# Kernel tuning notes

Measured on AMD Instinct MI355X. Metric: run time of the kernel, lower is better.

Reference implementation:

```python
import jax, jax.numpy as jnp
import numpy as np

B, S, D = 4, 4096, 1024
H, R = 16, 256
HD = D // H  # 64

def setup_inputs() -> dict:
    key = jax.random.key(0)
    ks = jax.random.split(key, 10)
    s = 1.0 / np.sqrt(D)
    return {
        "x": jax.random.normal(ks[0], (B, S, D), dtype=jnp.float32),
        "wq": jax.random.normal(ks[1], (D, D), dtype=jnp.float32) * s,
        "bq": jnp.zeros((D,), dtype=jnp.float32),
        "wk": jax.random.normal(ks[2], (D, D), dtype=jnp.float32) * s,
        "bk": jnp.zeros((D,), dtype=jnp.float32),
        "wv": jax.random.normal(ks[3], (D, D), dtype=jnp.float32) * s,
        "bv": jnp.zeros((D,), dtype=jnp.float32),
        "wo": jax.random.normal(ks[4], (D, D), dtype=jnp.float32) * s,
        "bo": jnp.zeros((D,), dtype=jnp.float32),
        "random_features": jax.random.normal(ks[5], (H, HD, R), dtype=jnp.float32),
    }

def reference(x, wq, bq, wk, bk, wv, bv, wo, bo, random_features):
    b, s, _ = x.shape
    # projections (torch Linear: x @ W.T + b) -> [b, h, s, hd]
    def proj(w, bias):
        return (x @ w.T + bias).reshape(b, s, H, HD).transpose(0, 2, 1, 3)
    q = proj(wq, bq)
    k = proj(wk, bk)
    v = proj(wv, bv)
    # random feature maps: [b,h,s,r]
    q_prime = jnp.exp(jnp.einsum('bhsd,hdr->bhsr', q, random_features)
                      - 0.5 * jnp.sum(q * q, axis=-1, keepdims=True))
    k_prime = jnp.exp(jnp.einsum('bhsd,hdr->bhsr', k, random_features)
                      - 0.5 * jnp.sum(k * k, axis=-1, keepdims=True))
    # kv aggregation: [b,h,r,hd]
    kv_prime = jnp.einsum('bhsr,bhsd->bhrd', k_prime, v)
    attn = jnp.einsum('bhsr,bhrd->bhsd', q_prime, kv_prime)
    # normalization: [b,h,s,1]
    norm = jnp.einsum('bhsr,bhr->bhs', q_prime, jnp.sum(k_prime, axis=-2))[..., None]
    attn = attn / (norm + 1e-6)
    attn = attn.transpose(0, 2, 1, 3).reshape(b, s, D)
    return attn @ wo.T + bo
```

## Files before the change

### kernel.cpp

```cpp
#include <hip/hip_runtime.h>
#include <stdint.h>

#define B_  4
#define S_  4096
#define D_  1024
#define H_  16
#define R_  256
#define HD_ 64
#define BH_ 64
#define M_  16384
#define SPLITK_ 8

typedef uint16_t u16;
typedef __attribute__((ext_vector_type(8))) short short8;
typedef __attribute__((ext_vector_type(4))) float f32x4;
typedef __attribute__((ext_vector_type(4))) unsigned short us4;

__device__ __forceinline__ u16 f2bf(float f){
  union { float f; uint32_t u; } v; v.f = f;
  uint32_t r = v.u + 0x7FFFu + ((v.u >> 16) & 1u);
  return (u16)(r >> 16);
}
__device__ __forceinline__ float bf2f(u16 h){
  union { uint32_t u; float f; } v; v.u = ((uint32_t)h) << 16;
  return v.f;
}
__device__ __forceinline__ f32x4 mfma16(short8 a, short8 b, f32x4 c){
  return __builtin_amdgcn_mfma_f32_16x16x32_bf16(a, b, c, 0, 0, 0);
}
__device__ __forceinline__ void gl_lds16(const u16* g, u16* l){
  __builtin_amdgcn_global_load_lds((const __attribute__((address_space(1))) void*)g,
                                   (__attribute__((address_space(3))) void*)l, 16, 0, 0);
}
__device__ __forceinline__ void cvt8(const float4& a, const float4& b, short8& hi, short8& lo){
  float f[8] = {a.x,a.y,a.z,a.w,b.x,b.y,b.z,b.w};
  #pragma unroll
  for (int j=0;j<8;j++){
    u16 h = f2bf(f[j]);
    hi[j] = (short)h;
    lo[j] = (short)f2bf(f[j] - bf2f(h));
  }
}

__device__ __forceinline__ void stage_rf_full(const u16* __restrict__ rfh,
                                              const u16* __restrict__ rfl,
                                              int h, int tid, int w,
                                              u16* lrfh, u16* lrfl){
  const u16* baseH = rfh + (size_t)h*(R_*HD_);
  const u16* baseL = rfl + (size_t)h*(R_*HD_);
  #pragma unroll
  for (int c=0;c<8;c++){
    int idx = c*256 + tid;
    int row = idx >> 3, gd = idx & 7;
    int gs  = gd ^ (row & 7);
    gl_lds16(baseH + row*64 + gs*8, lrfh + c*2048 + w*512);
    gl_lds16(baseL + row*64 + gs*8, lrfl + c*2048 + w*512);
  }
}

__device__ __forceinline__ void stage_rf_half(const u16* __restrict__ rfh,
                                              const u16* __restrict__ rfl,
                                              int h, int th, int tid, int w,
                                              u16* lrfh, u16* lrfl){
  const u16* baseH = rfh + (size_t)h*(R_*HD_) + (size_t)th*128*HD_;
  const u16* baseL = rfl + (size_t)h*(R_*HD_) + (size_t)th*128*HD_;
  #pragma unroll
  for (int c=0;c<4;c++){
    int idx = c*256 + tid;
    int row = idx >> 3, gd = idx & 7;
    int gs  = gd ^ (row & 7);
    gl_lds16(baseH + row*64 + gs*8, lrfh + c*2048 + w*512);
    gl_lds16(baseL + row*64 + gs*8, lrfl + c*2048 + w*512);
  }
}

__global__ void split_kernel(const float* __restrict__ src, u16* __restrict__ hi,
                             u16* __restrict__ lo, int n4){
  int i = blockIdx.x*blockDim.x + threadIdx.x;
  if (i >= n4) return;
  float4 f = ((const float4*)src)[i];
  float ff[4] = {f.x,f.y,f.z,f.w};
  us4 hv, lv;
  #pragma unroll
  for (int j=0;j<4;j++){
    u16 h = f2bf(ff[j]);
    hv[j] = h;
    lv[j] = f2bf(ff[j] - bf2f(h));
  }
  ((us4*)hi)[i] = hv;
  if (lo) ((us4*)lo)[i] = lv;
}

__global__ void rf_split_kernel(const float* __restrict__ rf, u16* __restrict__ rhi,
                                u16* __restrict__ rlo){
  int idx = blockIdx.x*256 + threadIdx.x;
  int d = idx & 63, r = (idx >> 6) & 255, h = idx >> 14;
  float f = rf[((size_t)h*HD_ + d)*R_ + r];
  u16 hh = f2bf(f);
  rhi[idx] = hh;
  rlo[idx] = f2bf(f - bf2f(hh));
}

__device__ __forceinline__ void rowsq(const float4& x0, const float4& x1,
                                      const float4& x2, const float4& x3,
                                      int q, float sql[4]){
  float s = x0.x*x0.x + x0.y*x0.y + x0.z*x0.z + x0.w*x0.w
          + x1.x*x1.x + x1.y*x1.y + x1.z*x1.z + x1.w*x1.w
          + x2.x*x2.x + x2.y*x2.y + x2.z*x2.z + x2.w*x2.w
          + x3.x*x3.x + x3.y*x3.y + x3.z*x3.z + x3.w*x3.w;
  s += __shfl_xor(s, 16);
  s += __shfl_xor(s, 32);
  #pragma unroll
  for (int r4=0;r4<4;r4++) sql[r4] = 0.5f * __shfl(s, q*4 + r4);
}

template<int NSPLIT, int EPI>
__global__ __launch_bounds__(256, 2)
void gemm128(const u16* __restrict__ Ah, const u16* __restrict__ Al,
             const u16* __restrict__ Bh, const u16* __restrict__ Bl,
             const float* __restrict__ bias, float* __restrict__ outF,
             u16* __restrict__ outB){
  constexpr int NBUF = (NSPLIT==3) ? 4 : 2;
  __shared__ u16 lds[NBUF * 4096];
  const int tid = threadIdx.x, w = tid >> 6, lane = tid & 63;
  const int wm = w & 1, wn = w >> 1;
  const int m0 = blockIdx.x * 128, n0 = blockIdx.y * 128;
  const int q = lane >> 4, rr = lane & 15;

  const int c0 = w*2, c1 = w*2 + 1;
  const int row0 = c0*16 + (lane >> 2), row1 = c1*16 + (lane >> 2);
  const int g0 = (lane & 3) ^ ((row0 >> 1) & 3);
  const int g1 = (lane & 3) ^ ((row1 >> 1) & 3);
  const size_t a0 = (size_t)(m0 + row0)*1024 + g0*8;
  const size_t a1 = (size_t)(m0 + row1)*1024 + g1*8;
  const size_t b0 = (size_t)(n0 + row0)*1024 + g0*8;
  const size_t b1 = (size_t)(n0 + row1)*1024 + g1*8;

  f32x4 acc[4][4];
  #pragma unroll
  for (int i=0;i<4;i++)
    #pragma unroll
    for (int j=0;j<4;j++) acc[i][j] = f32x4{0.f,0.f,0.f,0.f};

  for (int kt=0; kt<32; kt++){
    const int k0 = kt*32;
    gl_lds16(Ah + a0 + k0, lds + 0*4096 + c0*512);
    gl_lds16(Ah + a1 + k0, lds + 0*4096 + c1*512);
    gl_lds16(Bh + b0 + k0, lds + 1*4096 + c0*512);
    gl_lds16(Bh + b1 + k0, lds + 1*4096 + c1*512);
    if constexpr (NSPLIT == 3){
      gl_lds16(Al + a0 + k0, lds + 2*4096 + c0*512);
      gl_lds16(Al + a1 + k0, lds + 2*4096 + c1*512);
      gl_lds16(Bl + b0 + k0, lds + 3*4096 + c0*512);
      gl_lds16(Bl + b1 + k0, lds + 3*4096 + c1*512);
    }
    __syncthreads();

    short8 afh[4], bfh[4], afl[4], bfl[4];
    #pragma unroll
    for (int i=0;i<4;i++){
      int r  = wm*64 + i*16 + rr;
      int o  = r*32 + ((q ^ ((r >> 1) & 3))*8);
      afh[i] = *(const short8*)(lds + 0*4096 + o);
      if constexpr (NSPLIT == 3) afl[i] = *(const short8*)(lds + 2*4096 + o);
      int rn = wn*64 + i*16 + rr;
      int on = rn*32 + ((q ^ ((rn >> 1) & 3))*8);
      bfh[i] = *(const short8*)(lds + 1*4096 + on);
      if constexpr (NSPLIT == 3) bfl[i] = *(const short8*)(lds + 3*4096 + on);
    }
    #pragma unroll
    for (int i=0;i<4;i++)
      #pragma unroll
      for (int j=0;j<4;j++){
        acc[i][j] = mfma16(afh[i], bfh[j], acc[i][j]);
        if constexpr (NSPLIT == 3){
          acc[i][j] = mfma16(afh[i], bfl[j], acc[i][j]);
          acc[i][j] = mfma16(afl[i], bfh[j], acc[i][j]);
        }
      }
    __syncthreads();
  }

  #pragma unroll
  for (int i=0;i<4;i++){
    #pragma unroll
    for (int j=0;j<4;j++){
      int n  = n0 + wn*64 + j*16 + rr;
      float bb = bias[n];
      if constexpr (EPI == 1){
        int mb = m0 + wm*64 + i*16 + q*4;
        us4 pk;
        #pragma unroll
        for (int r4=0;r4<4;r4++) pk[r4] = f2bf(acc[i][j][r4] + bb);
        *(us4*)(outB + ((size_t)((mb >> 12)*H_ + (n >> 6))*HD_ + (n & 63))*S_ + (mb & 4095)) = pk;
      } else {
        #pragma unroll
        for (int r4=0;r4<4;r4++){
          int m = m0 + wm*64 + i*16 + q*4 + r4;
          float v = acc[i][j][r4] + bb;
          if constexpr (EPI == 0)
            outF[((size_t)((m >> 12)*H_ + (n >> 6)))*S_*HD_ + (size_t)(m & 4095)*HD_ + (n & 63)] = v;
          else
            outF[(size_t)m*1024 + n] = v;
        }
      }
    }
  }
}

__global__ __launch_bounds__(256, 1)
void kfeat_kv_kernel(const float* __restrict__ k32,
                     const u16* __restrict__ rfh, const u16* __restrict__ rfl,
                     const u16* __restrict__ vt, u16* __restrict__ kvp16){
  __shared__ u16 kp[128*72];
  __shared__ u16 lrfh[128*HD_];
  __shared__ u16 lrfl[128*HD_];
  const int sp = blockIdx.x, hb = blockIdx.y, th = blockIdx.z, h = hb & 15;
  const int tid = threadIdx.x, w = tid >> 6, lane = tid & 63;
  const int q = lane >> 4, rr = lane & 15;
  const int sw8 = rr & 7;

  stage_rf_half(rfh, rfl, h, th, tid, w, lrfh, lrfl);

  short8 ones;
  { u16 one = (rr == 0) ? (u16)0x3F80 : (u16)0;
    #pragma unroll
    for (int j=0;j<8;j++) ones[j] = (short)one; }

  f32x4 acc2[2][5];
  #pragma unroll
  for (int a=0;a<2;a++)
    #pragma unroll
    for (int t=0;t<5;t++) acc2[a][t] = f32x4{0.f,0.f,0.f,0.f};

  __syncthreads();

  const float* ap0 = k32 + ((size_t)hb*S_ + sp*(S_/SPLITK_) + w*16 + rr)*HD_ + q*8;
  float4 x0 = *(const float4*)(ap0);
  float4 x1 = *(const float4*)(ap0 + 4);
  float4 x2 = *(const float4*)(ap0 + 32);
  float4 x3 = *(const float4*)(ap0 + 36);

  for (int sub=0; sub<(S_/SPLITK_)/64; sub++){
    const int s0 = sp*(S_/SPLITK_) + sub*64;
    float sql[4];
    rowsq(x0, x1, x2, x3, q, sql);
    short8 ah[2], al[2];
    cvt8(x0, x1, ah[0], al[0]);
    cvt8(x2, x3, ah[1], al[1]);
    if (sub < (S_/SPLITK_)/64 - 1){
      const float* apn = k32 + ((size_t)hb*S_ + s0 + 64 + w*16 + rr)*HD_ + q*8;
      x0 = *(const float4*)(apn);
      x1 = *(const float4*)(apn + 4);
      x2 = *(const float4*)(apn + 32);
      x3 = *(const float4*)(apn + 36);
    }

    f32x4 accp[8];
    #pragma unroll
    for (int tt=0;tt<8;tt++) accp[tt] = f32x4{0.f,0.f,0.f,0.f};
    #pragma unroll
    for (int tt=0;tt<8;tt++){
      const u16* lrow  = lrfh + (tt*16 + rr)*64;
      const u16* lrowl = lrfl + (tt*16 + rr)*64;
      short8 bh0 = *(const short8*)(lrow  + ((q     ^ sw8))*8);
      short8 bh1 = *(const short8*)(lrow  + (((q+4) ^ sw8))*8);
      short8 bl0 = *(const short8*)(lrowl + ((q     ^ sw8))*8);
      short8 bl1 = *(const short8*)(lrowl + (((q+4) ^ sw8))*8);
      f32x4 c = accp[tt];
      c = mfma16(ah[0], bh0, c); c = mfma16(ah[0], bl0, c); c = mfma16(al[0], bh0, c);
      c = mfma16(ah[1], bh1, c); c = mfma16(ah[1], bl1, c); c = mfma16(al[1], bh1, c);
      accp[tt] = c;
    }
    #pragma unroll
    for (int tt=0;tt<8;tt++){
      us4 pk;
      #pragma unroll
      for (int r4=0;r4<4;r4++) pk[r4] = f2bf(__expf(accp[tt][r4] - sql[r4]));
      *(us4*)(kp + (tt*16 + rr)*72 + w*16 + q*4) = pk;
    }
    __syncthreads();
    #pragma unroll
    for (int ks=0; ks<2; ks++){
      short8 af[2];
      #pragma unroll
      for (int a=0;a<2;a++)
        af[a] = *(const short8*)(kp + (w*32 + a*16 + rr)*72 + ks*32 + q*8);
      #pragma unroll
      for (int t=0;t<5;t++){
        short8 bf;
        if (t < 4)
          bf = *(const short8*)(vt + ((size_t)hb*HD_ + t*16 + rr)*S_ + s0 + ks*32 + q*8);
        else
          bf = ones;
        #pragma unroll
        for (int a=0;a<2;a++) acc2[a][t] = mfma16(af[a], bf, acc2[a][t]);
      }
    }
    __syncthreads();
  }
  u16* op = kvp16 + ((size_t)hb*SPLITK_ + sp)*R_*80;
  #pragma unroll
  for (int a=0;a<2;a++)
    #pragma unroll
    for (int t=0;t<5;t++)
      #pragma unroll
      for (int r4=0;r4<4;r4++){
        int r = th*128 + w*32 + a*16 + q*4 + r4;
        int c = t*16 + rr;
        op[r*80 + c] = f2bf(acc2[a][t][r4]);
      }
}

__global__ void kv_reduce_kernel(const u16* __restrict__ kvp16, u16* __restrict__ kvt,
                                 float* __restrict__ ksum){
  int r = blockIdx.x, hb = blockIdx.y, c = threadIdx.x;
  if (c >= 65) return;
  const u16* base = kvp16 + (size_t)hb*SPLITK_*R_*80 + r*80 + c;
  float s = 0.f;
  #pragma unroll
  for (int sp=0; sp<SPLITK_; sp++) s += bf2f(base[(size_t)sp*R_*80]);
  if (c < 64) kvt[((size_t)hb*HD_ + c)*R_ + r] = f2bf(s);
  else        ksum[(size_t)hb*R_ + r] = s;
}

__global__ __launch_bounds__(256, 1)
void qfeat_attn_kernel(const float* __restrict__ q32,
                       const u16* __restrict__ rfh, const u16* __restrict__ rfl,
                       const u16* __restrict__ kvt, const float* __restrict__ ksum,
                       u16* __restrict__ attn_c){
  __shared__ u16 qp[64*264];
  __shared__ u16 lrfh[R_*HD_];
  __shared__ u16 lrfl[R_*HD_];
  __shared__ u16 lkvt[HD_*R_];
  const int sc8 = blockIdx.x, hb = blockIdx.y, h = hb & 15, b = hb >> 4;
  const int tid = threadIdx.x, w = tid >> 6, lane = tid & 63;
  const int q = lane >> 4, rr = lane & 15;
  const int sw8 = rr & 7;

  stage_rf_full(rfh, rfl, h, tid, w, lrfh, lrfl);
  {
    const u16* kg = kvt + (size_t)hb*HD_*R_;
    #pragma unroll
    for (int c=0;c<8;c++){
      int idx = c*256 + tid;
      int row = idx >> 5, gd = idx & 31;
      int gs  = gd ^ (row & 7);
      gl_lds16(kg + row*256 + gs*8, lkvt + c*2048 + w*512);
    }
  }

  float kslv[16];
  #pragma unroll
  for (int t=0;t<16;t++) kslv[t] = ksum[(size_t)hb*R_ + t*16 + rr];

  __syncthreads();

  const float* ap0 = q32 + ((size_t)hb*S_ + sc8*512 + w*16 + rr)*HD_ + q*8;
  float4 x0 = *(const float4*)(ap0);
  float4 x1 = *(const float4*)(ap0 + 4);
  float4 x2 = *(const float4*)(ap0 + 32);
  float4 x3 = *(const float4*)(ap0 + 36);

  for (int sub=0; sub<8; sub++){
    const int s0 = sc8*512 + sub*64;
    float sql[4];
    rowsq(x0, x1, x2, x3, q, sql);
    short8 ah[2], al[2];
    cvt8(x0, x1, ah[0], al[0]);
    cvt8(x2, x3, ah[1], al[1]);
    if (sub < 7){
      const float* apn = q32 + ((size_t)hb*S_ + s0 + 64 + w*16 + rr)*HD_ + q*8;
      x0 = *(const float4*)(apn);
      x1 = *(const float4*)(apn + 4);
      x2 = *(const float4*)(apn + 32);
      x3 = *(const float4*)(apn + 36);
    }

    f32x4 accp[16];
    #pragma unroll
    for (int t=0;t<16;t++) accp[t] = f32x4{0.f,0.f,0.f,0.f};
    #pragma unroll
    for (int t=0;t<16;t++){
      const u16* lrow  = lrfh + (t*16 + rr)*64;
      const u16* lrowl = lrfl + (t*16 + rr)*64;
      short8 bh0 = *(const short8*)(lrow  + ((q     ^ sw8))*8);
      short8 bh1 = *(const short8*)(lrow  + (((q+4) ^ sw8))*8);
      short8 bl0 = *(const short8*)(lrowl + ((q     ^ sw8))*8);
      short8 bl1 = *(const short8*)(lrowl + (((q+4) ^ sw8))*8);
      f32x4 c = accp[t];
      c = mfma16(ah[0], bh0, c); c = mfma16(ah[0], bl0, c); c = mfma16(al[0], bh0, c);
      c = mfma16(ah[1], bh1, c); c = mfma16(ah[1], bl1, c); c = mfma16(al[1], bh1, c);
      accp[t] = c;
    }
    float npl[4] = {0.f, 0.f, 0.f, 0.f};
    #pragma unroll
    for (int t=0;t<16;t++){
      us4 pk;
      #pragma unroll
      for (int r4=0;r4<4;r4++){
        float e = __expf(accp[t][r4] - sql[r4]);
        npl[r4] += e * kslv[t];
        pk[r4] = f2bf(e);
      }
      #pragma unroll
      for (int r4=0;r4<4;r4++)
        qp[(w*16 + q*4 + r4)*264 + t*16 + rr] = pk[r4];
    }
    #pragma unroll
    for (int r4=0;r4<4;r4++){
      npl[r4] += __shfl_xor(npl[r4], 1);
      npl[r4] += __shfl_xor(npl[r4], 2);
      npl[r4] += __shfl_xor(npl[r4], 4);
      npl[r4] += __shfl_xor(npl[r4], 8);
    }

    f32x4 acc[4];
    #pragma unroll
    for (int t=0;t<4;t++) acc[t] = f32x4{0.f,0.f,0.f,0.f};
    #pragma unroll
    for (int ks=0; ks<8; ks++){
      short8 af = *(const short8*)(qp + (w*16 + rr)*264 + ks*32 + q*8);
      #pragma unroll
      for (int t=0;t<4;t++){
        short8 bf = *(const short8*)(lkvt + (t*16 + rr)*256 + (((ks*4 + q) ^ sw8))*8);
        acc[t] = mfma16(af, bf, acc[t]);
      }
    }

    #pragma unroll
    for (int t=0;t<4;t++)
      #pragma unroll
      for (int r4=0;r4<4;r4++){
        int sl = w*16 + q*4 + r4;
        int d  = t*16 + rr;
        float o = acc[t][r4] / (npl[r4] + 1e-6f);
        attn_c[((size_t)b*S_ + s0 + sl)*D_ + h*HD_ + d] = f2bf(o);
      }
  }
}

extern "C" void kernel_launch(void* const* d_in, const int* in_sizes, int n_in,
                              void* d_out, int out_size, void* d_ws, size_t ws_size,
                              hipStream_t stream){
  (void)in_sizes; (void)n_in; (void)out_size; (void)ws_size;
  const float* x  = (const float*)d_in[0];
  const float* wq = (const float*)d_in[1];
  const float* bq = (const float*)d_in[2];
  const float* wk = (const float*)d_in[3];
  const float* bk = (const float*)d_in[4];
  const float* wv = (const float*)d_in[5];
  const float* bv = (const float*)d_in[6];
  const float* wo = (const float*)d_in[7];
  const float* bo = (const float*)d_in[8];
  const float* rf = (const float*)d_in[9];
  float* out = (float*)d_out;

  char* p = (char*)d_ws;
  size_t off = 0;
  auto take = [&](size_t bytes)->char*{
    char* r = p + off; off += (bytes + 255) & ~(size_t)255; return r;
  };
  u16*  x_hi  = (u16*)take((size_t)M_*D_*2);
  u16*  x_lo  = (u16*)take((size_t)M_*D_*2);
  u16*  wq_hi = (u16*)take((size_t)D_*D_*2);
  u16*  wq_lo = (u16*)take((size_t)D_*D_*2);
  u16*  wk_hi = (u16*)take((size_t)D_*D_*2);
  u16*  wk_lo = (u16*)take((size_t)D_*D_*2);
  u16*  wv_hi = (u16*)take((size_t)D_*D_*2);
  u16*  wo_hi = (u16*)take((size_t)D_*D_*2);
  u16*  rf_hi = (u16*)take((size_t)H_*R_*HD_*2);
  u16*  rf_lo = (u16*)take((size_t)H_*R_*HD_*2);
  float* q32  = (float*)take((size_t)M_*D_*4);
  float* k32  = (float*)take((size_t)M_*D_*4);
  u16*  v_t   = (u16*)take((size_t)M_*D_*2);
  u16*  kvt   = (u16*)take((size_t)BH_*HD_*R_*2);
  float* ksum = (float*)take((size_t)BH_*R_*4);
  u16* attn_c = x_hi;
  u16* kvp16  = x_lo;

  split_kernel<<<dim3((M_*D_)/1024), 256, 0, stream>>>(x,  x_hi,  x_lo,  (M_*D_)/4);
  split_kernel<<<dim3((D_*D_)/1024), 256, 0, stream>>>(wq, wq_hi, wq_lo, (D_*D_)/4);
  split_kernel<<<dim3((D_*D_)/1024), 256, 0, stream>>>(wk, wk_hi, wk_lo, (D_*D_)/4);
  split_kernel<<<dim3((D_*D_)/1024), 256, 0, stream>>>(wv, wv_hi, nullptr, (D_*D_)/4);
  split_kernel<<<dim3((D_*D_)/1024), 256, 0, stream>>>(wo, wo_hi, nullptr, (D_*D_)/4);
  rf_split_kernel<<<dim3((H_*R_*HD_)/256), 256, 0, stream>>>(rf, rf_hi, rf_lo);

  gemm128<3,0><<<dim3(M_/128, D_/128), 256, 0, stream>>>(x_hi, x_lo, wq_hi, wq_lo, bq, q32, nullptr);
  gemm128<3,0><<<dim3(M_/128, D_/128), 256, 0, stream>>>(x_hi, x_lo, wk_hi, wk_lo, bk, k32, nullptr);
  gemm128<1,1><<<dim3(M_/128, D_/128), 256, 0, stream>>>(x_hi, nullptr, wv_hi, nullptr, bv, nullptr, v_t);

  kfeat_kv_kernel<<<dim3(SPLITK_, BH_, 2), 256, 0, stream>>>(k32, rf_hi, rf_lo, v_t, kvp16);
  kv_reduce_kernel<<<dim3(R_, BH_), 128, 0, stream>>>(kvp16, kvt, ksum);

  qfeat_attn_kernel<<<dim3(8, BH_), 256, 0, stream>>>(q32, rf_hi, rf_lo, kvt, ksum, attn_c);

  gemm128<1,2><<<dim3(M_/128, D_/128), 256, 0, stream>>>(attn_c, nullptr, wo_hi, nullptr, bo, out, nullptr);
}
```

Measured before the change: 595.5 us.

## Fuse Q/K projections into one GEMM and merge prep splits into one kernel

Concatenates wq and wk into a single 2048-wide weight so one split-bf16 GEMM produces both Q and K into an interleaved [b, 32, s, hd] buffer. All input-splitting kernels (x, weights, random features) and a bias concat are merged into a single prep launch. The Q-feature attention kernel now handles 1024 rows per block with 4 blocks per head instead of 8. This removes several launches and gives the projection GEMM a bigger grid, but halves the parallelism of the Q-attention stage (256 blocks), which may underfill the GPU.

```diff
diff --git a/kernel.cpp b/kernel.cpp
--- a/kernel.cpp
+++ b/kernel.cpp
@@ -74,10 +74,12 @@
   }
 }
 
-__global__ void split_kernel(const float* __restrict__ src, u16* __restrict__ hi,
-                             u16* __restrict__ lo, int n4){
-  int i = blockIdx.x*blockDim.x + threadIdx.x;
-  if (i >= n4) return;
+#define XB_ ((M_*D_)/1024)
+#define WB_ ((D_*D_)/1024)
+__device__ __forceinline__ void split_body(const float* __restrict__ src,
+                                           u16* __restrict__ hi, u16* __restrict__ lo,
+                                           int bid, int tid){
+  int i = bid*256 + tid;
   float4 f = ((const float4*)src)[i];
   float ff[4] = {f.x,f.y,f.z,f.w};
   us4 hv, lv;
@@ -90,15 +92,39 @@
   ((us4*)hi)[i] = hv;
   if (lo) ((us4*)lo)[i] = lv;
 }
-
-__global__ void rf_split_kernel(const float* __restrict__ rf, u16* __restrict__ rhi,
-                                u16* __restrict__ rlo){
-  int idx = blockIdx.x*256 + threadIdx.x;
-  int d = idx & 63, r = (idx >> 6) & 255, h = idx >> 14;
-  float f = rf[((size_t)h*HD_ + d)*R_ + r];
-  u16 hh = f2bf(f);
-  rhi[idx] = hh;
-  rlo[idx] = f2bf(f - bf2f(hh));
+__global__ void prep_kernel(const float* __restrict__ x,  const float* __restrict__ wq,
+                            const float* __restrict__ wk, const float* __restrict__ wv,
+                            const float* __restrict__ wo, const float* __restrict__ rf,
+                            const float* __restrict__ bq, const float* __restrict__ bk,
+                            u16* __restrict__ x_hi, u16* __restrict__ x_lo,
+                            u16* __restrict__ wqk_hi, u16* __restrict__ wqk_lo,
+                            u16* __restrict__ wv_hi, u16* __restrict__ wo_hi,
+                            u16* __restrict__ rf_hi, u16* __restrict__ rf_lo,
+                            float* __restrict__ bqk){
+  int bid = blockIdx.x, tid = threadIdx.x;
+  if (bid < XB_){ split_body(x, x_hi, x_lo, bid, tid); return; }
+  bid -= XB_;
+  if (bid < WB_){ split_body(wq, wqk_hi, wqk_lo, bid, tid); return; }
+  bid -= WB_;
+  if (bid < WB_){ split_body(wk, wqk_hi + (size_t)D_*D_, wqk_lo + (size_t)D_*D_, bid, tid); return; }
+  bid -= WB_;
+  if (bid < WB_){ split_body(wv, wv_hi, nullptr, bid, tid); return; }
+  bid -= WB_;
+  if (bid < WB_){ split_body(wo, wo_hi, nullptr, bid, tid); return; }
+  bid -= WB_;
+  if (bid < 1024){
+    int idx = bid*256 + tid;
+    int d = idx & 63, r = (idx >> 6) & 255, h = idx >> 14;
+    float f = rf[((size_t)h*HD_ + d)*R_ + r];
+    u16 hh = f2bf(f);
+    rf_hi[idx] = hh;
+    rf_lo[idx] = f2bf(f - bf2f(hh));
+    return;
+  }
+  bid -= 1024;
+  int i = bid*256 + tid;
+  if (i < 1024)       bqk[i] = bq[i];
+  else if (i < 2048)  bqk[i] = bk[i - 1024];
 }
 
 __device__ __forceinline__ void rowsq(const float4& x0, const float4& x1,
@@ -199,7 +225,7 @@
           int m = m0 + wm*64 + i*16 + q*4 + r4;
           float v = acc[i][j][r4] + bb;
           if constexpr (EPI == 0)
-            outF[((size_t)((m >> 12)*H_ + (n >> 6)))*S_*HD_ + (size_t)(m & 4095)*HD_ + (n & 63)] = v;
+            outF[((size_t)((m >> 12)*32 + (n >> 6)))*S_*HD_ + (size_t)(m & 4095)*HD_ + (n & 63)] = v;
           else
             outF[(size_t)m*1024 + n] = v;
         }
@@ -209,7 +235,7 @@
 }
 
 __global__ __launch_bounds__(256, 1)
-void kfeat_kv_kernel(const float* __restrict__ k32,
+void kfeat_kv_kernel(const float* __restrict__ qk32,
                      const u16* __restrict__ rfh, const u16* __restrict__ rfl,
                      const u16* __restrict__ vt, u16* __restrict__ kvp16){
   __shared__ u16 kp[128*72];
@@ -219,6 +245,7 @@
   const int tid = threadIdx.x, w = tid >> 6, lane = tid & 63;
   const int q = lane >> 4, rr = lane & 15;
   const int sw8 = rr & 7;
+  const float* kbp = qk32 + (size_t)((hb >> 4)*32 + 16 + h)*S_*HD_;
 
   stage_rf_half(rfh, rfl, h, th, tid, w, lrfh, lrfl);
 
@@ -235,7 +262,7 @@
 
   __syncthreads();
 
-  const float* ap0 = k32 + ((size_t)hb*S_ + sp*(S_/SPLITK_) + w*16 + rr)*HD_ + q*8;
+  const float* ap0 = kbp + (size_t)(sp*(S_/SPLITK_) + w*16 + rr)*HD_ + q*8;
   float4 x0 = *(const float4*)(ap0);
   float4 x1 = *(const float4*)(ap0 + 4);
   float4 x2 = *(const float4*)(ap0 + 32);
@@ -249,7 +276,7 @@
     cvt8(x0, x1, ah[0], al[0]);
     cvt8(x2, x3, ah[1], al[1]);
     if (sub < (S_/SPLITK_)/64 - 1){
-      const float* apn = k32 + ((size_t)hb*S_ + s0 + 64 + w*16 + rr)*HD_ + q*8;
+      const float* apn = kbp + (size_t)(s0 + 64 + w*16 + rr)*HD_ + q*8;
       x0 = *(const float4*)(apn);
       x1 = *(const float4*)(apn + 4);
       x2 = *(const float4*)(apn + 32);
@@ -325,7 +352,7 @@
 }
 
 __global__ __launch_bounds__(256, 1)
-void qfeat_attn_kernel(const float* __restrict__ q32,
+void qfeat_attn_kernel(const float* __restrict__ qk32,
                        const u16* __restrict__ rfh, const u16* __restrict__ rfl,
                        const u16* __restrict__ kvt, const float* __restrict__ ksum,
                        u16* __restrict__ attn_c){
@@ -333,10 +360,11 @@
   __shared__ u16 lrfh[R_*HD_];
   __shared__ u16 lrfl[R_*HD_];
   __shared__ u16 lkvt[HD_*R_];
-  const int sc8 = blockIdx.x, hb = blockIdx.y, h = hb & 15, b = hb >> 4;
+  const int sc = blockIdx.x, hb = blockIdx.y, h = hb & 15, b = hb >> 4;
   const int tid = threadIdx.x, w = tid >> 6, lane = tid & 63;
   const int q = lane >> 4, rr = lane & 15;
   const int sw8 = rr & 7;
+  const float* qbp = qk32 + (size_t)(b*32 + h)*S_*HD_;
 
   stage_rf_full(rfh, rfl, h, tid, w, lrfh, lrfl);
   {
@@ -356,21 +384,21 @@
 
   __syncthreads();
 
-  const float* ap0 = q32 + ((size_t)hb*S_ + sc8*512 + w*16 + rr)*HD_ + q*8;
+  const float* ap0 = qbp + (size_t)(sc*1024 + w*16 + rr)*HD_ + q*8;
   float4 x0 = *(const float4*)(ap0);
   float4 x1 = *(const float4*)(ap0 + 4);
   float4 x2 = *(const float4*)(ap0 + 32);
   float4 x3 = *(const float4*)(ap0 + 36);
 
-  for (int sub=0; sub<8; sub++){
-    const int s0 = sc8*512 + sub*64;
+  for (int sub=0; sub<16; sub++){
+    const int s0 = sc*1024 + sub*64;
     float sql[4];
     rowsq(x0, x1, x2, x3, q, sql);
     short8 ah[2], al[2];
     cvt8(x0, x1, ah[0], al[0]);
     cvt8(x2, x3, ah[1], al[1]);
-    if (sub < 7){
-      const float* apn = q32 + ((size_t)hb*S_ + s0 + 64 + w*16 + rr)*HD_ + q*8;
+    if (sub < 15){
+      const float* apn = qbp + (size_t)(s0 + 64 + w*16 + rr)*HD_ + q*8;
       x0 = *(const float4*)(apn);
       x1 = *(const float4*)(apn + 4);
       x2 = *(const float4*)(apn + 32);
@@ -461,39 +489,33 @@
   auto take = [&](size_t bytes)->char*{
     char* r = p + off; off += (bytes + 255) & ~(size_t)255; return r;
   };
-  u16*  x_hi  = (u16*)take((size_t)M_*D_*2);
-  u16*  x_lo  = (u16*)take((size_t)M_*D_*2);
-  u16*  wq_hi = (u16*)take((size_t)D_*D_*2);
-  u16*  wq_lo = (u16*)take((size_t)D_*D_*2);
-  u16*  wk_hi = (u16*)take((size_t)D_*D_*2);
-  u16*  wk_lo = (u16*)take((size_t)D_*D_*2);
-  u16*  wv_hi = (u16*)take((size_t)D_*D_*2);
-  u16*  wo_hi = (u16*)take((size_t)D_*D_*2);
-  u16*  rf_hi = (u16*)take((size_t)H_*R_*HD_*2);
-  u16*  rf_lo = (u16*)take((size_t)H_*R_*HD_*2);
-  float* q32  = (float*)take((size_t)M_*D_*4);
-  float* k32  = (float*)take((size_t)M_*D_*4);
-  u16*  v_t   = (u16*)take((size_t)M_*D_*2);
-  u16*  kvt   = (u16*)take((size_t)BH_*HD_*R_*2);
-  float* ksum = (float*)take((size_t)BH_*R_*4);
+  u16*  x_hi   = (u16*)take((size_t)M_*D_*2);
+  u16*  x_lo   = (u16*)take((size_t)M_*D_*2);
+  u16*  wqk_hi = (u16*)take((size_t)2*D_*D_*2);
+  u16*  wqk_lo = (u16*)take((size_t)2*D_*D_*2);
+  u16*  wv_hi  = (u16*)take((size_t)D_*D_*2);
+  u16*  wo_hi  = (u16*)take((size_t)D_*D_*2);
+  u16*  rf_hi  = (u16*)take((size_t)H_*R_*HD_*2);
+  u16*  rf_lo  = (u16*)take((size_t)H_*R_*HD_*2);
+  float* bqk   = (float*)take((size_t)2048*4);
+  float* qk32  = (float*)take((size_t)M_*2048*4);
+  u16*  v_t    = (u16*)take((size_t)M_*D_*2);
+  u16*  kvt    = (u16*)take((size_t)BH_*HD_*R_*2);
+  float* ksum  = (float*)take((size_t)BH_*R_*4);
   u16* attn_c = x_hi;
   u16* kvp16  = x_lo;
 
-  split_kernel<<<dim3((M_*D_)/1024), 256, 0, stream>>>(x,  x_hi,  x_lo,  (M_*D_)/4);
-  split_kernel<<<dim3((D_*D_)/1024), 256, 0, stream>>>(wq, wq_hi, wq_lo, (D_*D_)/4);
-  split_kernel<<<dim3((D_*D_)/1024), 256, 0, stream>>>(wk, wk_hi, wk_lo, (D_*D_)/4);
-  split_kernel<<<dim3((D_*D_)/1024), 256, 0, stream>>>(wv, wv_hi, nullptr, (D_*D_)/4);
-  split_kernel<<<dim3((D_*D_)/1024), 256, 0, stream>>>(wo, wo_hi, nullptr, (D_*D_)/4);
-  rf_split_kernel<<<dim3((H_*R_*HD_)/256), 256, 0, stream>>>(rf, rf_hi, rf_lo);
-
-  gemm128<3,0><<<dim3(M_/128, D_/128), 256, 0, stream>>>(x_hi, x_lo, wq_hi, wq_lo, bq, q32, nullptr);
-  gemm128<3,0><<<dim3(M_/128, D_/128), 256, 0, stream>>>(x_hi, x_lo, wk_hi, wk_lo, bk, k32, nullptr);
+  prep_kernel<<<dim3(XB_ + 4*WB_ + 1024 + 8), 256, 0, stream>>>(
+      x, wq, wk, wv, wo, rf, bq, bk,
+      x_hi, x_lo, wqk_hi, wqk_lo, wv_hi, wo_hi, rf_hi, rf_lo, bqk);
+
+  gemm128<3,0><<<dim3(M_/128, 2048/128), 256, 0, stream>>>(x_hi, x_lo, wqk_hi, wqk_lo, bqk, qk32, nullptr);
   gemm128<1,1><<<dim3(M_/128, D_/128), 256, 0, stream>>>(x_hi, nullptr, wv_hi, nullptr, bv, nullptr, v_t);
 
-  kfeat_kv_kernel<<<dim3(SPLITK_, BH_, 2), 256, 0, stream>>>(k32, rf_hi, rf_lo, v_t, kvp16);
+  kfeat_kv_kernel<<<dim3(SPLITK_, BH_, 2), 256, 0, stream>>>(qk32, rf_hi, rf_lo, v_t, kvp16);
   kv_reduce_kernel<<<dim3(R_, BH_), 128, 0, stream>>>(kvp16, kvt, ksum);
 
-  qfeat_attn_kernel<<<dim3(8, BH_), 256, 0, stream>>>(q32, rf_hi, rf_lo, kvt, ksum, attn_c);
+  qfeat_attn_kernel<<<dim3(4, BH_), 256, 0, stream>>>(qk32, rf_hi, rf_lo, kvt, ksum, attn_c);
 
   gemm128<1,2><<<dim3(M_/128, D_/128), 256, 0, stream>>>(attn_c, nullptr, wo_hi, nullptr, bo, out, nullptr);
 }
```

Measured after the change: 589.1 us. Within noise of the previous version (-1.1%).
